# Performance work log

Measured on AMD Instinct MI355X. Metric: run time of the kernel, lower is better.

Reference implementation:

```python
import jax, jax.numpy as jnp
import numpy as np

# NF4 codebook used by bitsandbytes Linear4bit (quant_type='nf4')
NF4_CODE = jnp.array([
    -1.0, -0.6961928009986877, -0.5250730514526367, -0.39491748809814453,
    -0.28444138169288635, -0.18477343022823334, -0.09105003625154495, 0.0,
    0.07958029955625534, 0.16093020141124725, 0.24611230194568634,
    0.33791524171829224, 0.44070982933044434, 0.5626170039176941,
    0.7229568362236023, 1.0], dtype=jnp.float32)

SCALE = 32.0 / 16.0  # alpha / r


def setup_inputs() -> dict:
    key = jax.random.key(0)
    k1, k2, k3, k4, k5 = jax.random.split(key, 5)
    B, S, IN, OUT, R = 4, 2048, 4096, 4096, 16
    BLK = 64  # Linear4bit default blocksize
    x = jax.random.normal(k1, (B, S, IN), dtype=jnp.float32)
    w_codes = jax.random.randint(k2, (OUT, IN), 0, 16, dtype=jnp.int32)
    absmax = jax.random.uniform(k3, (OUT, IN // BLK), dtype=jnp.float32)
    W_a = jax.random.normal(k4, (IN, R), dtype=jnp.float32)
    W_b = jax.random.normal(k5, (R, OUT), dtype=jnp.float32)
    return {"x": x, "w_codes": w_codes, "absmax": absmax, "W_a": W_a, "W_b": W_b}


def reference(x, w_codes, absmax, W_a, W_b):
    out_f, in_f = w_codes.shape
    blocks = absmax.shape[1]
    # NF4 dequantize: codebook lookup * per-block absmax scale  -> W [out, in]
    W = (NF4_CODE[w_codes].reshape(out_f, blocks, -1)
         * absmax[:, :, None]).reshape(out_f, in_f).astype(x.dtype)
    # quantized linear (no bias)
    y = jnp.einsum('bsi,oi->bso', x, W)
    # LoRA low-rank update: scale * (x @ W_a @ W_b)
    y = y + SCALE * ((x @ W_a.astype(x.dtype)) @ W_b.astype(x.dtype))
    return y
```

## Files before the change

kernel.cpp:

```cpp
#include <hip/hip_runtime.h>
#include <hip/hip_bf16.h>
#include <stdint.h>

#define IN_F 4096
#define OUT_F 4096
#define RANK 16
#define LORA_SCALE 2.0f

typedef __attribute__((ext_vector_type(8))) short short8;
typedef __attribute__((ext_vector_type(4))) float f32x4;
typedef __attribute__((ext_vector_type(16))) float f32x16;

__device__ __constant__ float NF4_CODE[16] = {
    -1.0f, -0.6961928009986877f, -0.5250730514526367f, -0.39491748809814453f,
    -0.28444138169288635f, -0.18477343022823334f, -0.09105003625154495f, 0.0f,
    0.07958029955625534f, 0.16093020141124725f, 0.24611230194568634f,
    0.33791524171829224f, 0.44070982933044434f, 0.5626170039176941f,
    0.7229568362236023f, 1.0f};

__device__ __forceinline__ short bf16_rne(float f) {
    uint32_t u = __builtin_bit_cast(uint32_t, f);
    u += 0x7fffu + ((u >> 16) & 1u);
    return (short)(u >> 16);
}

__device__ __forceinline__ void load_lds16(const short* g, short* l) {
    __builtin_amdgcn_global_load_lds(
        (const __attribute__((address_space(1))) void*)g,
        (__attribute__((address_space(3))) void*)l, 16, 0, 0);
}

__global__ __launch_bounds__(256)
void prep_kernel(const int* __restrict__ codes, const float* __restrict__ am,
                 const float* __restrict__ Wa, const float* __restrict__ Wb,
                 const float* __restrict__ x, short* __restrict__ Weff,
                 short* __restrict__ xb)
{
    const int tid = threadIdx.x;

    if (blockIdx.x >= 4096) {
        const size_t i = (size_t)(blockIdx.x - 4096) * 256 + tid;
        const f32x4* xv = (const f32x4*)x;
        f32x4 a = xv[2 * i], b = xv[2 * i + 1];
        short8 o;
        o[0] = bf16_rne(a[0]); o[1] = bf16_rne(a[1]);
        o[2] = bf16_rne(a[2]); o[3] = bf16_rne(a[3]);
        o[4] = bf16_rne(b[0]); o[5] = bf16_rne(b[1]);
        o[6] = bf16_rne(b[2]); o[7] = bf16_rne(b[3]);
        ((short8*)xb)[i] = o;
        return;
    }

    __shared__ float WaT[RANK * 64];
    __shared__ float Wbs[RANK * 64];

    const int iBase = (blockIdx.x & 63) * 64;
    const int oBase = (blockIdx.x >> 6) * 64;

    {
        f32x4 v = *(const f32x4*)(Wa + (size_t)iBase * RANK + tid * 4);
        #pragma unroll
        for (int j = 0; j < 4; j++) {
            int e = tid * 4 + j;
            WaT[(e & 15) * 64 + (e >> 4)] = v[j];
        }
        int r = tid >> 4, c = (tid & 15) * 4;
        f32x4 w = *(const f32x4*)(Wb + (size_t)r * OUT_F + oBase + c);
        *(f32x4*)&Wbs[r * 64 + c] = w;
    }
    __syncthreads();

    #pragma unroll
    for (int p = 0; p < 2; p++) {
        const int g  = tid + p * 256;
        const int o  = g >> 3;
        const int ig = (g & 7) * 8;
        const float amax = am[(size_t)(oBase + o) * (IN_F / 64) + (iBase >> 6)];

        const int4* cp = (const int4*)(codes + (size_t)(oBase + o) * IN_F + iBase + ig);
        int4 c0 = cp[0], c1 = cp[1];
        int cc[8] = {c0.x, c0.y, c0.z, c0.w, c1.x, c1.y, c1.z, c1.w};

        float acc[8] = {0, 0, 0, 0, 0, 0, 0, 0};
        #pragma unroll
        for (int r = 0; r < RANK; r++) {
            float wb = Wbs[r * 64 + o];
            f32x4 a0 = *(const f32x4*)&WaT[r * 64 + ig];
            f32x4 a1 = *(const f32x4*)&WaT[r * 64 + ig + 4];
            acc[0] += a0[0] * wb;  acc[1] += a0[1] * wb;
            acc[2] += a0[2] * wb;  acc[3] += a0[3] * wb;
            acc[4] += a1[0] * wb;  acc[5] += a1[1] * wb;
            acc[6] += a1[2] * wb;  acc[7] += a1[3] * wb;
        }

        short8 out;
        #pragma unroll
        for (int j = 0; j < 8; j++)
            out[j] = bf16_rne(NF4_CODE[cc[j] & 15] * amax + LORA_SCALE * acc[j]);
        *(short8*)(Weff + (size_t)(oBase + o) * IN_F + iBase + ig) = out;
    }
}

template<bool ABF16>
__global__ __launch_bounds__(256)
void gemm32(const void* __restrict__ Ain, const short* __restrict__ Bt,
            float* __restrict__ C)
{
    __shared__ __align__(16) short lds[16384];
    short* sA = lds;
    short* sB = lds + 8192;

    const int tid  = threadIdx.x;
    const int lane = tid & 63;
    const int wave = tid >> 6;
    const int mBase = blockIdx.y * 128;
    const int nBase = blockIdx.x * 128;
    const int wm = (wave >> 1) * 64;
    const int wn = (wave & 1) * 64;

    const int srow = tid >> 3;
    const int scol = ((tid & 7) ^ (srow & 7)) * 8;

    const short* gA[4]; const float* fA[4]; const short* gB[4];
    #pragma unroll
    for (int p = 0; p < 4; p++) {
        if constexpr (ABF16)
            gA[p] = (const short*)Ain + (size_t)(mBase + p * 32 + srow) * IN_F + scol;
        else
            fA[p] = (const float*)Ain + (size_t)(mBase + p * 32 + srow) * IN_F + scol;
        gB[p] = Bt + (size_t)(nBase + p * 32 + srow) * IN_F + scol;
    }
    short* dA[4]; short* dB[4];
    #pragma unroll
    for (int p = 0; p < 4; p++) {
        dA[p] = sA + (p * 256 + tid) * 8;
        dB[p] = sB + (p * 256 + tid) * 8;
    }

    const int l31 = lane & 31;
    const int h   = lane >> 5;
    const int r7  = lane & 7;
    int xo[4];
    #pragma unroll
    for (int s = 0; s < 4; s++) xo[s] = ((s * 2 + h) ^ r7) * 8;
    const int rA0 = (wm + l31) * 64, rA1 = rA0 + 32 * 64;
    const int rB0 = (wn + l31) * 64, rB1 = rB0 + 32 * 64;

    f32x16 acc[2][2];
    #pragma unroll
    for (int i = 0; i < 2; i++)
        #pragma unroll
        for (int j = 0; j < 2; j++)
            #pragma unroll
            for (int r = 0; r < 16; r++)
                acc[i][j][r] = 0.f;

    for (int k0 = 0; k0 < IN_F; k0 += 64) {
        if constexpr (ABF16) {
            #pragma unroll
            for (int p = 0; p < 4; p++) load_lds16(gA[p] + k0, dA[p]);
        } else {
            #pragma unroll
            for (int p = 0; p < 4; p++) {
                const float* s0 = fA[p] + k0;
                f32x4 v0 = *(const f32x4*)s0;
                f32x4 v1 = *(const f32x4*)(s0 + 4);
                short8 o;
                #pragma unroll
                for (int j = 0; j < 4; j++) {
                    o[j] = bf16_rne(v0[j]); o[j + 4] = bf16_rne(v1[j]);
                }
                *(short8*)dA[p] = o;
            }
        }
        #pragma unroll
        for (int p = 0; p < 4; p++) load_lds16(gB[p] + k0, dB[p]);
        __syncthreads();

        #pragma unroll
        for (int s = 0; s < 4; s++) {
            short8 a0 = *(const short8*)(sA + rA0 + xo[s]);
            short8 a1 = *(const short8*)(sA + rA1 + xo[s]);
            short8 b0 = *(const short8*)(sB + rB0 + xo[s]);
            short8 b1 = *(const short8*)(sB + rB1 + xo[s]);
            acc[0][0] = __builtin_amdgcn_mfma_f32_32x32x16_bf16(a0, b0, acc[0][0], 0, 0, 0);
            acc[0][1] = __builtin_amdgcn_mfma_f32_32x32x16_bf16(a0, b1, acc[0][1], 0, 0, 0);
            acc[1][0] = __builtin_amdgcn_mfma_f32_32x32x16_bf16(a1, b0, acc[1][0], 0, 0, 0);
            acc[1][1] = __builtin_amdgcn_mfma_f32_32x32x16_bf16(a1, b1, acc[1][1], 0, 0, 0);
        }
        __syncthreads();
    }

    #pragma unroll
    for (int mi = 0; mi < 2; mi++) {
        #pragma unroll
        for (int ni = 0; ni < 2; ni++) {
            const int col  = nBase + wn + ni * 32 + l31;
            const int rowb = mBase + wm + mi * 32 + 4 * h;
            #pragma unroll
            for (int r = 0; r < 16; r++) {
                const int row = rowb + (r & 3) + 8 * (r >> 2);
                C[(size_t)row * OUT_F + col] = acc[mi][ni][r];
            }
        }
    }
}

extern "C" void kernel_launch(void* const* d_in, const int* in_sizes, int n_in,
                              void* d_out, int out_size, void* d_ws, size_t ws_size,
                              hipStream_t stream)
{
    const float* x     = (const float*)d_in[0];
    const int*   codes = (const int*)d_in[1];
    const float* am    = (const float*)d_in[2];
    const float* Wa    = (const float*)d_in[3];
    const float* Wb    = (const float*)d_in[4];
    float* out = (float*)d_out;

    const int M = in_sizes[0] / IN_F;

    short* Weff = (short*)d_ws;
    short* xb   = Weff + (size_t)OUT_F * IN_F;
    const size_t need_full =
        ((size_t)OUT_F * IN_F + (size_t)M * IN_F) * sizeof(short);

    if (ws_size >= need_full) {
        const int castBlocks = (M * IN_F / 8) / 256;
        prep_kernel<<<4096 + castBlocks, 256, 0, stream>>>(
            codes, am, Wa, Wb, x, Weff, xb);
        gemm32<true><<<dim3(OUT_F / 128, M / 128), 256, 0, stream>>>(
            xb, Weff, out);
    } else {
        prep_kernel<<<4096, 256, 0, stream>>>(
            codes, am, Wa, Wb, x, Weff, Weff );
        gemm32<false><<<dim3(OUT_F / 128, M / 128), 256, 0, stream>>>(
            x, Weff, out);
    }
}
```

Baseline: 551.8 us.

## Add 256x256-tile double-buffered bf16 GEMM with phased MFMA/load pipeline

Adds a new GEMM kernel with 256x256 output tiles, 512 threads, double-buffered 128KB LDS, and an eight-phase schedule. Each phase issues async global-to-LDS loads for future k-tiles while running 16x16x32 MFMAs on the current quadrant, using explicit barriers, waitcnt and setprio. It also remaps block ids into groups of eight for L2 locality. The aim is to raise arithmetic intensity and hide memory latency compared with the single-buffered 128x128 kernel, at the cost of high register and LDS use and fragile hand-written synchronization.

```diff
diff --git a/kernel.cpp b/kernel.cpp
--- a/kernel.cpp
+++ b/kernel.cpp
@@ -206,6 +206,154 @@
     }
 }
 
+#define FENCE() __builtin_amdgcn_sched_barrier(0)
+#define BARRIER() do { asm volatile("" ::: "memory"); FENCE(); \
+    __builtin_amdgcn_s_barrier(); FENCE(); asm volatile("" ::: "memory"); } while(0)
+#define WAIT_LGKM0() do { asm volatile("s_waitcnt lgkmcnt(0)" ::: "memory"); FENCE(); } while(0)
+#define WAIT_VM6() do { asm volatile("s_waitcnt vmcnt(6)" ::: "memory"); FENCE(); } while(0)
+
+#define STAGE_A(BUF, H, T) do { \
+    const short* _g = gA + (size_t)(H) * 128 * IN_F + (T) * 64; \
+    load_lds16(_g,                   lds + (BUF)*32768 + (H)*8192 + tid*8); \
+    load_lds16(_g + (size_t)64*IN_F, lds + (BUF)*32768 + (H)*8192 + 4096 + tid*8); \
+} while(0)
+
+#define STAGE_B(BUF, H, T) do { \
+    const short* _g = gB + (size_t)(H) * 128 * IN_F + (T) * 64; \
+    load_lds16(_g,                   lds + (BUF)*32768 + 16384 + (H)*8192 + tid*8); \
+    load_lds16(_g + (size_t)64*IN_F, lds + (BUF)*32768 + 16384 + (H)*8192 + 4096 + tid*8); \
+} while(0)
+
+#define READ_A(BUF, MQ) do { \
+    const short* _s = lds + (BUF)*32768 + (MQ)*8192; \
+    _Pragma("unroll") \
+    for (int mf = 0; mf < 4; ++mf) { \
+        const int row = wm*64 + mf*16 + l15; \
+        const short* _r = _s + row*64; \
+        const int rs = row & 7; \
+        afr[mf][0] = *(const short8*)(_r + ((kl     ) ^ rs) * 8); \
+        afr[mf][1] = *(const short8*)(_r + ((kl | 4) ^ rs) * 8); \
+    } \
+} while(0)
+
+#define READ_B(BUF, NQ) do { \
+    const short* _s = lds + (BUF)*32768 + 16384 + (NQ)*8192; \
+    _Pragma("unroll") \
+    for (int nf = 0; nf < 2; ++nf) { \
+        const int row = wn*32 + nf*16 + l15; \
+        const short* _r = _s + row*64; \
+        const int rs = row & 7; \
+        bfr[nf][0] = *(const short8*)(_r + ((kl     ) ^ rs) * 8); \
+        bfr[nf][1] = *(const short8*)(_r + ((kl | 4) ^ rs) * 8); \
+    } \
+} while(0)
+
+#define MFMA_QUAD(MQ, NQ) do { \
+    _Pragma("unroll") \
+    for (int ks = 0; ks < 2; ++ks) \
+    _Pragma("unroll") \
+    for (int mf = 0; mf < 4; ++mf) \
+    _Pragma("unroll") \
+    for (int nf = 0; nf < 2; ++nf) \
+        acc[MQ][NQ][mf][nf] = __builtin_amdgcn_mfma_f32_16x16x32_bf16( \
+            afr[mf][ks], bfr[nf][ks], acc[MQ][NQ][mf][nf], 0, 0, 0); \
+} while(0)
+
+#define PHASE(RDA, RDB, BUF, MQ, NQ, STAGE_STMT, VM_STMT) do { \
+    if (RDA) READ_A(BUF, MQ); \
+    if (RDB) READ_B(BUF, NQ); \
+    STAGE_STMT; \
+    BARRIER(); \
+    WAIT_LGKM0(); \
+    __builtin_amdgcn_s_setprio(1); \
+    MFMA_QUAD(MQ, NQ); \
+    __builtin_amdgcn_s_setprio(0); \
+    VM_STMT; \
+    BARRIER(); \
+} while(0)
+
+__global__ __launch_bounds__(512, 2)
+void gemm256(const short* __restrict__ A, const short* __restrict__ Bt,
+             float* __restrict__ C)
+{
+    __shared__ __align__(16) short lds[65536];
+
+    const int tid  = threadIdx.x;
+    const int lane = tid & 63;
+    const int wave = tid >> 6;
+    const int wm  = wave >> 2;
+    const int wn  = wave & 3;
+    const int l15 = lane & 15;
+    const int kl  = lane >> 4;
+
+    const int nwg = gridDim.x;
+    int bid = blockIdx.x;
+    bid = (bid & 7) * (nwg >> 3) + (bid >> 3);
+    const int by = bid >> 4;
+    const int bx = bid & 15;
+    const int mBase = by * 256;
+    const int nBase = bx * 256;
+
+    const int rt = tid >> 3;
+    const int sw = ((tid & 7) ^ (rt & 7)) * 8;
+    const short* gA = A  + (size_t)(mBase + rt) * IN_F + sw;
+    const short* gB = Bt + (size_t)(nBase + rt) * IN_F + sw;
+
+    f32x4 acc[2][2][4][2];
+    #pragma unroll
+    for (int i = 0; i < 2; ++i)
+    #pragma unroll
+    for (int j = 0; j < 2; ++j)
+    #pragma unroll
+    for (int m = 0; m < 4; ++m)
+    #pragma unroll
+    for (int n = 0; n < 2; ++n)
+    #pragma unroll
+    for (int r = 0; r < 4; ++r)
+        acc[i][j][m][n][r] = 0.f;
+
+    short8 afr[4][2];
+    short8 bfr[2][2];
+
+    STAGE_A(0, 0, 0); STAGE_B(0, 1, 0); STAGE_A(0, 1, 0); STAGE_B(0, 0, 0);
+    STAGE_A(1, 0, 1); STAGE_B(1, 1, 1); STAGE_A(1, 1, 1);
+    WAIT_VM6();
+    BARRIER();
+
+    const int NT = IN_F / 64;
+    #pragma unroll 1
+    for (int it = 0; it < NT / 2; ++it) {
+        const int T  = 2 * it;
+        const int t2 = (T + 2 < NT) ? (T + 2) : (NT - 1);
+        const int t3 = (T + 3 < NT) ? (T + 3) : (NT - 1);
+        PHASE(1, 1, 0, 0, 0, STAGE_B(1, 0, T + 1), (void)0);
+        PHASE(0, 1, 0, 0, 1, STAGE_A(0, 0, t2),    (void)0);
+        PHASE(1, 0, 0, 1, 1, STAGE_B(0, 1, t2),    (void)0);
+        PHASE(0, 1, 0, 1, 0, STAGE_A(0, 1, t2),    WAIT_VM6());
+        PHASE(1, 1, 1, 0, 0, STAGE_B(0, 0, t2),    (void)0);
+        PHASE(0, 1, 1, 0, 1, STAGE_A(1, 0, t3),    (void)0);
+        PHASE(1, 0, 1, 1, 1, STAGE_B(1, 1, t3),    (void)0);
+        PHASE(0, 1, 1, 1, 0, STAGE_A(1, 1, t3),    WAIT_VM6());
+    }
+
+    #pragma unroll
+    for (int mq = 0; mq < 2; ++mq)
+    #pragma unroll
+    for (int nq = 0; nq < 2; ++nq)
+    #pragma unroll
+    for (int mf = 0; mf < 4; ++mf) {
+        const int row0 = mBase + mq * 128 + wm * 64 + mf * 16 + kl * 4;
+        #pragma unroll
+        for (int nf = 0; nf < 2; ++nf) {
+            const int col = nBase + nq * 128 + wn * 32 + nf * 16 + l15;
+            float* cp = C + (size_t)row0 * OUT_F + col;
+            #pragma unroll
+            for (int r = 0; r < 4; ++r)
+                cp[(size_t)r * OUT_F] = acc[mq][nq][mf][nf][r];
+        }
+    }
+}
+
 extern "C" void kernel_launch(void* const* d_in, const int* in_sizes, int n_in,
                               void* d_out, int out_size, void* d_ws, size_t ws_size,
                               hipStream_t stream)
@@ -228,8 +376,13 @@
         const int castBlocks = (M * IN_F / 8) / 256;
         prep_kernel<<<4096 + castBlocks, 256, 0, stream>>>(
             codes, am, Wa, Wb, x, Weff, xb);
-        gemm32<true><<<dim3(OUT_F / 128, M / 128), 256, 0, stream>>>(
-            xb, Weff, out);
+        if ((M & 255) == 0) {
+            gemm256<<<dim3((OUT_F / 256) * (M / 256)), 512, 0, stream>>>(
+                xb, Weff, out);
+        } else {
+            gemm32<true><<<dim3(OUT_F / 128, M / 128), 256, 0, stream>>>(
+                xb, Weff, out);
+        }
     } else {
         prep_kernel<<<4096, 256, 0, stream>>>(
             codes, am, Wa, Wb, x, Weff, Weff );
```

New measurement: 484.0 us. -12.3%, faster.
